# Kernel optimization log

Measured on AMD Instinct MI355X. Metric: run time of the kernel, lower is better.

Reference implementation:

```python
import jax, jax.numpy as jnp
import numpy as np

B, P, O, C = 32, 65536, 32, 2
THRESH = 0.35
VAR = (0.1, 0.2)
LOC_W, LANDM_W = 2.0, 1.0
ALPHA, GAMMA = 0.25, 1.5
EPS = 1e-7


def setup_inputs():
    key = jax.random.key(0)
    k = jax.random.split(key, 8)
    loc_data = jax.random.normal(k[0], (B, P, 4), jnp.float32) * 0.1
    conf_data = jax.random.normal(k[1], (B, P, C), jnp.float32)
    landm_data = jax.random.normal(k[2], (B, P, 10), jnp.float32) * 0.1
    # priors in center form (cx, cy, w, h)
    cxcy = jax.random.uniform(k[3], (P, 2), minval=0.05, maxval=0.95)
    wh = jax.random.uniform(k[4], (P, 2), minval=0.02, maxval=0.3)
    priors = jnp.concatenate([cxcy, wh], axis=-1).astype(jnp.float32)
    # targets [B, O, 15]: corner box (4) + 5 landmarks (10) + label (1, in {-1, +1})
    xy1 = jax.random.uniform(k[5], (B, O, 2), minval=0.0, maxval=0.7)
    bwh = jax.random.uniform(k[6], (B, O, 2), minval=0.05, maxval=0.25)
    boxes = jnp.concatenate([xy1, xy1 + bwh], axis=-1)
    landms = jnp.tile(xy1 + bwh * 0.5, (1, 1, 5))
    labels = (jax.random.randint(k[7], (B, O, 1), 0, 2) * 2 - 1).astype(jnp.float32)
    targets = jnp.concatenate([boxes, landms, labels], axis=-1)
    return {"loc_data": loc_data, "conf_data": conf_data, "landm_data": landm_data,
            "priors": priors, "targets": targets}


def point_form(pr):  # (cx,cy,w,h) -> (x1,y1,x2,y2)
    return jnp.concatenate([pr[:, :2] - pr[:, 2:] / 2, pr[:, :2] + pr[:, 2:] / 2], -1)


def pairwise_iou(a, b):  # a [O,4], b [P,4] corner form -> [O,P]
    lt = jnp.maximum(a[:, None, :2], b[None, :, :2])
    rb = jnp.minimum(a[:, None, 2:], b[None, :, 2:])
    whd = jnp.clip(rb - lt, 0.0)
    inter = whd[..., 0] * whd[..., 1]
    area_a = ((a[:, 2] - a[:, 0]) * (a[:, 3] - a[:, 1]))[:, None]
    area_b = ((b[:, 2] - b[:, 0]) * (b[:, 3] - b[:, 1]))[None, :]
    return inter / (area_a + area_b - inter)


def encode_landm(matched, priors):  # matched [P,10], priors [P,4] center form
    m = matched.reshape(P, 5, 2)
    g = (m - priors[:, None, :2]) / (VAR[0] * priors[:, None, 2:])
    return g.reshape(P, 10)


def match_one(truths, landms, labels, priors_pf, priors):
    ov = pairwise_iou(truths, priors_pf)                       # [O,P]
    best_prior_idx = jnp.argmax(ov, axis=1)                    # [O] best prior per gt
    best_truth_overlap = ov.max(axis=0)                        # [P]
    best_truth_idx = jnp.argmax(ov, axis=0)                    # [P]
    # ensure every gt keeps its best prior
    best_truth_overlap = best_truth_overlap.at[best_prior_idx].set(2.0)
    best_truth_idx = best_truth_idx.at[best_prior_idx].set(jnp.arange(truths.shape[0]))
    loc_t = truths[best_truth_idx]                             # [P,4] matched gt boxes (corner)
    conf = jnp.where(best_truth_overlap < THRESH, 0.0, labels[best_truth_idx])
    landm_t = encode_landm(landms[best_truth_idx], priors)     # [P,10]
    return loc_t, conf, landm_t


def decode(loc, priors):  # SSD center-form decode -> corner boxes
    xy = priors[..., :2] + loc[..., :2] * VAR[0] * priors[..., 2:]
    wh = priors[..., 2:] * jnp.exp(loc[..., 2:] * VAR[1])
    return jnp.concatenate([xy - wh / 2, xy + wh / 2], -1)


def giou(b1, b2):  # elementwise GIoU, corner form
    area1 = (b1[..., 2] - b1[..., 0]) * (b1[..., 3] - b1[..., 1])
    area2 = (b2[..., 2] - b2[..., 0]) * (b2[..., 3] - b2[..., 1])
    iw = jnp.clip(jnp.minimum(b1[..., 2], b2[..., 2]) - jnp.maximum(b1[..., 0], b2[..., 0]), 0.0)
    ih = jnp.clip(jnp.minimum(b1[..., 3], b2[..., 3]) - jnp.maximum(b1[..., 1], b2[..., 1]), 0.0)
    inter = iw * ih
    union = area1 + area2 - inter
    iou = inter / (union + EPS)
    ew = jnp.maximum(b1[..., 2], b2[..., 2]) - jnp.minimum(b1[..., 0], b2[..., 0])
    eh = jnp.maximum(b1[..., 3], b2[..., 3]) - jnp.minimum(b1[..., 1], b2[..., 1])
    enc = ew * eh
    return iou - (enc - union) / (enc + EPS)


def smooth_l1(x):
    ax = jnp.abs(x)
    return jnp.where(ax < 1.0, 0.5 * x * x, ax - 0.5)


def reference(loc_data, conf_data, landm_data, priors, targets):
    # matching uses detached (.data) priors/targets in the original
    priors_c = jax.lax.stop_gradient(priors)
    targets_c = jax.lax.stop_gradient(targets)
    truths, landms, labels = targets_c[..., :4], targets_c[..., 4:14], targets_c[..., 14]
    priors_pf = point_form(priors_c)
    loc_t, conf_raw, landm_t = jax.vmap(match_one, in_axes=(0, 0, 0, None, None))(
        truths, landms, labels, priors_pf, priors_c)  # [B,P,4],[B,P],[B,P,10]

    # landmark loss on pos1 = conf > 0 (label +1: face with landmarks)
    pos1 = conf_raw > 0
    N1 = jnp.maximum(pos1.sum().astype(jnp.float32), 1.0)
    loss_landm = (smooth_l1(landm_data - landm_t).sum(-1) * pos1).sum() * LANDM_W

    # loc GIoU loss on pos = conf != 0
    pos = conf_raw != 0
    conf_t = pos.astype(jnp.int32)  # conf_t[pos] = 1, background 0
    dec = decode(loc_data, priors_c[None])  # [B,P,4]
    loss_l = jnp.where(pos, 1.0 - giou(dec, loc_t), 0.0).sum() * LOC_W

    # focal loss over all B*P anchors (size_average=False -> sum)
    logp = jax.nn.log_softmax(conf_data, axis=-1)
    logp_t = jnp.take_along_axis(logp, conf_t[..., None], axis=-1)[..., 0]
    p_t = jnp.exp(logp_t)
    loss_c = (-ALPHA * (1.0 - p_t) ** GAMMA * logp_t).sum()

    # original normalizes loss_l and loss_c by num_pos_landm sum (N), landm by N1 (==N)
    N = N1
    return (loss_l / N, loss_c / N, loss_landm / N1)
```

## Files before the change

### kernel.cpp

```cpp
#include <hip/hip_runtime.h>
#include <cstdint>

#define B_ 32
#define P_ 65536
#define O_ 32
#define GX_ 64
#define KC_ 4
#define THRESH_ 0.35f
#define VAR0 0.1f
#define VAR1 0.2f
#define EPS_ 1e-7f
#define ALPHA_ 0.25f

struct WSHdr {
  unsigned long long gkey[B_ * O_];
  float4 part[GX_ * B_];
};

__device__ __forceinline__ float frcp(float x) { return __builtin_amdgcn_rcpf(x); }

template <int CTRL>
__device__ __forceinline__ float dpp_fmax(float v) {
  int s = __builtin_amdgcn_update_dpp(0, __float_as_int(v), CTRL, 0xF, 0xF, true);
  return fmaxf(v, __int_as_float(s));
}
template <int CTRL>
__device__ __forceinline__ unsigned dpp_umax(unsigned v) {
  unsigned u = (unsigned)__builtin_amdgcn_update_dpp(0, (int)v, CTRL, 0xF, 0xF, true);
  return u > v ? u : v;
}

__global__ void init_ws(WSHdr* ws) {
  int t = blockIdx.x * blockDim.x + threadIdx.x;
  if (t < B_ * O_) ws->gkey[t] = 0ull;
}

template <bool BIG>
__global__ __launch_bounds__(256) void k_match(const float* __restrict__ priors,
                                               const float* __restrict__ targets,
                                               WSHdr* __restrict__ ws,
                                               uint2* __restrict__ pb) {
  __shared__ float tsh[O_][5];
  __shared__ unsigned long long kq[O_][17];
  const int b = blockIdx.y;
  const int tid = threadIdx.x;
  const int lane = tid & 63, wid = tid >> 6;
  if (tid < O_) {
    const float* trow = targets + ((size_t)b * O_ + tid) * 15;
    float x1 = trow[0], y1 = trow[1], x2 = trow[2], y2 = trow[3];
    tsh[tid][0] = x1; tsh[tid][1] = y1; tsh[tid][2] = x2; tsh[tid][3] = y2;
    tsh[tid][4] = (x2 - x1) * (y2 - y1);
  }
  __syncthreads();

  float px1[KC_], py1[KC_], px2[KC_], py2[KC_], pa[KC_], bov[KC_];
  int bidx[KC_];
  unsigned pinv[KC_];
  #pragma unroll
  for (int k = 0; k < KC_; ++k) {
    unsigned p = (unsigned)((blockIdx.x + k * GX_) * 256 + tid);
    pinv[k] = 0xFFFFFFFFu - p;
    float4 pr = reinterpret_cast<const float4*>(priors)[p];
    px1[k] = pr.x - pr.z * 0.5f; py1[k] = pr.y - pr.w * 0.5f;
    px2[k] = pr.x + pr.z * 0.5f; py2[k] = pr.y + pr.w * 0.5f;
    pa[k] = (px2[k] - px1[k]) * (py2[k] - py1[k]);
    bov[k] = -1.f; bidx[k] = 0;
  }

  #pragma unroll 4
  for (int o = 0; o < O_; ++o) {
    const float x1 = tsh[o][0], y1 = tsh[o][1], x2 = tsh[o][2], y2 = tsh[o][3];
    const float ta = tsh[o][4];
    float tiou = 0.f;
    unsigned tinv = pinv[0];
    #pragma unroll
    for (int k = 0; k < KC_; ++k) {
      float iw = fmaxf(fminf(x2, px2[k]) - fmaxf(x1, px1[k]), 0.f);
      float ih = fmaxf(fminf(y2, py2[k]) - fmaxf(y1, py1[k]), 0.f);
      float inter = iw * ih;
      float iou = inter * frcp(ta + pa[k] - inter);
      if (iou > bov[k]) { bov[k] = iou; bidx[k] = o; }
      if (iou > tiou)   { tiou = iou; tinv = pinv[k]; }
    }
    float m = tiou;
    m = dpp_fmax<0x128>(m);
    m = dpp_fmax<0x124>(m);
    m = dpp_fmax<0x122>(m);
    m = dpp_fmax<0x121>(m);
    unsigned cand = (tiou == m) ? tinv : 0u;
    cand = dpp_umax<0x128>(cand);
    cand = dpp_umax<0x124>(cand);
    cand = dpp_umax<0x122>(cand);
    cand = dpp_umax<0x121>(cand);
    if ((lane & 15) == 0)
      kq[o][wid * 4 + (lane >> 4)] =
          ((unsigned long long)__float_as_uint(m) << 32) | (unsigned long long)cand;
  }

  if (BIG) {
    #pragma unroll
    for (int k = 0; k < KC_; ++k)
      pb[(size_t)b * P_ + (0xFFFFFFFFu - pinv[k])] =
          make_uint2(__float_as_uint(bov[k]), (unsigned)bidx[k]);
  }
  __syncthreads();
  if (tid < O_) {
    unsigned long long best = kq[tid][0];
    #pragma unroll
    for (int s = 1; s < 16; ++s) {
      unsigned long long v = kq[tid][s];
      if (v > best) best = v;
    }
    atomicMax(&ws->gkey[(size_t)b * O_ + tid], best);
  }
}

template <bool BIG>
__global__ __launch_bounds__(256) void k_loss(const float* __restrict__ loc_data,
                                              const float* __restrict__ conf_data,
                                              const float* __restrict__ landm_data,
                                              const float* __restrict__ priors,
                                              const float* __restrict__ targets,
                                              WSHdr* __restrict__ ws,
                                              const uint2* __restrict__ pb) {
  __shared__ float tx1[O_], ty1[O_], tx2[O_], ty2[O_], tarea[O_], tlbl[O_];
  __shared__ float tlm[O_][10];
  __shared__ unsigned fp_s[O_];
  __shared__ unsigned char fmap[KC_ * 256];
  __shared__ float4 wsum[4];
  const int b = blockIdx.y;
  const int tid = threadIdx.x;
  #pragma unroll
  for (int k = 0; k < KC_; ++k) fmap[k * 256 + tid] = 0xFF;
  if (tid < O_) {
    const float* trow = targets + ((size_t)b * O_ + tid) * 15;
    float x1 = trow[0], y1 = trow[1], x2 = trow[2], y2 = trow[3];
    tx1[tid] = x1; ty1[tid] = y1; tx2[tid] = x2; ty2[tid] = y2;
    tarea[tid] = (x2 - x1) * (y2 - y1);
    #pragma unroll
    for (int k = 0; k < 10; ++k) tlm[tid][k] = trow[4 + k];
    tlbl[tid] = trow[14];
    fp_s[tid] = 0xFFFFFFFFu - (unsigned)(ws->gkey[(size_t)b * O_ + tid] & 0xFFFFFFFFull);
  }
  __syncthreads();
  if (tid == 0) {
    for (int j = 0; j < O_; ++j) {
      unsigned fp = fp_s[j];
      unsigned c = fp >> 8;
      if ((c & (GX_ - 1)) == (unsigned)blockIdx.x)
        fmap[(c >> 6) * 256 + (fp & 255)] = (unsigned char)j;
    }
  }
  __syncthreads();

  float vx = 0.f, vy = 0.f, vz = 0.f, vw = 0.f;

  #pragma unroll
  for (int k = 0; k < KC_; ++k) {
    const int p = (blockIdx.x + k * GX_) * 256 + tid;
    const size_t bp = (size_t)b * P_ + p;
    float4 pr = reinterpret_cast<const float4*>(priors)[p];

    float ov;
    int idx;
    if (BIG) {
      uint2 v = pb[bp];
      ov = __uint_as_float(v.x);
      idx = (int)v.y;
    } else {
      float px1 = pr.x - pr.z * 0.5f, py1 = pr.y - pr.w * 0.5f;
      float px2 = pr.x + pr.z * 0.5f, py2 = pr.y + pr.w * 0.5f;
      float parea = (px2 - px1) * (py2 - py1);
      float bov = -1.f;
      int bidx = 0;
      #pragma unroll 8
      for (int o = 0; o < O_; ++o) {
        float iw = fmaxf(fminf(tx2[o], px2) - fmaxf(tx1[o], px1), 0.f);
        float ih = fmaxf(fminf(ty2[o], py2) - fmaxf(ty1[o], py1), 0.f);
        float inter = iw * ih;
        float iou = inter * frcp(tarea[o] + parea - inter);
        if (iou > bov) { bov = iou; bidx = o; }
      }
      ov = bov; idx = bidx;
    }
    unsigned char fj = fmap[k * 256 + tid];
    if (fj != 0xFF) { idx = (int)fj; ov = 2.0f; }

    const bool pos = !(ov < THRESH_);
    const bool pos1 = pos && (tlbl[idx] > 0.f);

    float2 cf = reinterpret_cast<const float2*>(conf_data)[bp];
    float mx = fmaxf(cf.x, cf.y);
    float lse = mx + __logf(1.f + __expf(-fabsf(cf.x - cf.y)));
    float logpt = (pos ? cf.y : cf.x) - lse;
    float pt = __expf(logpt);
    float om = 1.f - pt;
    vy += -ALPHA_ * om * sqrtf(om) * logpt;

    if (pos) {
      float4 loc = reinterpret_cast<const float4*>(loc_data)[bp];
      float dx = pr.x + loc.x * VAR0 * pr.z;
      float dy = pr.y + loc.y * VAR0 * pr.w;
      float dw = pr.z * __expf(loc.z * VAR1);
      float dh = pr.w * __expf(loc.w * VAR1);
      float b1x1 = dx - dw * 0.5f, b1y1 = dy - dh * 0.5f;
      float b1x2 = dx + dw * 0.5f, b1y2 = dy + dh * 0.5f;
      float b2x1 = tx1[idx], b2y1 = ty1[idx], b2x2 = tx2[idx], b2y2 = ty2[idx];
      float a1 = (b1x2 - b1x1) * (b1y2 - b1y1);
      float a2 = (b2x2 - b2x1) * (b2y2 - b2y1);
      float iw = fmaxf(fminf(b1x2, b2x2) - fmaxf(b1x1, b2x1), 0.f);
      float ih = fmaxf(fminf(b1y2, b2y2) - fmaxf(b1y1, b2y1), 0.f);
      float inter = iw * ih;
      float uni = a1 + a2 - inter;
      float iou = inter * frcp(uni + EPS_);
      float ew = fmaxf(b1x2, b2x2) - fminf(b1x1, b2x1);
      float eh = fmaxf(b1y2, b2y2) - fminf(b1y1, b2y1);
      float enc = ew * eh;
      float g = iou - (enc - uni) * frcp(enc + EPS_);
      vx += 1.f - g;
    }
    if (pos1) {
      vw += 1.f;
      const float* lmrow = landm_data + bp * 10;
      float rw = frcp(VAR0 * pr.z);
      float rh = frcp(VAR0 * pr.w);
      float llm = 0.f;
      #pragma unroll
      for (int q = 0; q < 5; ++q) {
        float2 d = *reinterpret_cast<const float2*>(lmrow + q * 2);
        float ex = d.x - (tlm[idx][2 * q] - pr.x) * rw;
        float ey = d.y - (tlm[idx][2 * q + 1] - pr.y) * rh;
        float ax = fabsf(ex), ay = fabsf(ey);
        llm += (ax < 1.f) ? 0.5f * ex * ex : ax - 0.5f;
        llm += (ay < 1.f) ? 0.5f * ey * ey : ay - 0.5f;
      }
      vz += llm;
    }
  }

  #pragma unroll
  for (int i = 32; i > 0; i >>= 1) {
    vx += __shfl_xor(vx, i);
    vy += __shfl_xor(vy, i);
    vz += __shfl_xor(vz, i);
    vw += __shfl_xor(vw, i);
  }
  const int wave = tid >> 6, lane = tid & 63;
  if (lane == 0) wsum[wave] = make_float4(vx, vy, vz, vw);
  __syncthreads();
  if (tid == 0) {
    float sx = 0.f, sy = 0.f, sz = 0.f, sw = 0.f;
    #pragma unroll
    for (int w = 0; w < 4; ++w) {
      sx += wsum[w].x; sy += wsum[w].y; sz += wsum[w].z; sw += wsum[w].w;
    }
    ws->part[(size_t)blockIdx.y * GX_ + blockIdx.x] = make_float4(sx, sy, sz, sw);
  }
}

__global__ __launch_bounds__(256) void k_final(const WSHdr* __restrict__ ws,
                                               float* __restrict__ out) {
  __shared__ double sh[4][4];
  const int tid = threadIdx.x;
  double sx = 0.0, sy = 0.0, sz = 0.0, sw = 0.0;
  for (int i = tid; i < GX_ * B_; i += 256) {
    float4 v = ws->part[i];
    sx += v.x; sy += v.y; sz += v.z; sw += v.w;
  }
  #pragma unroll
  for (int i = 32; i > 0; i >>= 1) {
    sx += __shfl_xor(sx, i);
    sy += __shfl_xor(sy, i);
    sz += __shfl_xor(sz, i);
    sw += __shfl_xor(sw, i);
  }
  const int wave = tid >> 6, lane = tid & 63;
  if (lane == 0) { sh[wave][0] = sx; sh[wave][1] = sy; sh[wave][2] = sz; sh[wave][3] = sw; }
  __syncthreads();
  if (tid == 0) {
    double ax = 0, ay = 0, az = 0, aw = 0;
    #pragma unroll
    for (int w = 0; w < 4; ++w) { ax += sh[w][0]; ay += sh[w][1]; az += sh[w][2]; aw += sh[w][3]; }
    double n1 = aw < 1.0 ? 1.0 : aw;
    out[0] = (float)(2.0 * ax / n1);
    out[1] = (float)(ay / n1);
    out[2] = (float)(az / n1);
  }
}

extern "C" void kernel_launch(void* const* d_in, const int* in_sizes, int n_in,
                              void* d_out, int out_size, void* d_ws, size_t ws_size,
                              hipStream_t stream) {
  (void)in_sizes; (void)n_in; (void)out_size;
  const float* loc     = (const float*)d_in[0];
  const float* conf    = (const float*)d_in[1];
  const float* landm   = (const float*)d_in[2];
  const float* priors  = (const float*)d_in[3];
  const float* targets = (const float*)d_in[4];
  WSHdr* ws = (WSHdr*)d_ws;
  uint2* pb = (uint2*)((char*)d_ws + sizeof(WSHdr));
  float* out = (float*)d_out;
  const bool big = ws_size >= sizeof(WSHdr) + (size_t)B_ * P_ * sizeof(uint2);

  hipLaunchKernelGGL(init_ws, dim3(4), dim3(256), 0, stream, ws);
  dim3 grid(GX_, B_);
  if (big) {
    hipLaunchKernelGGL(k_match<true>, grid, dim3(256), 0, stream, priors, targets, ws, pb);
    hipLaunchKernelGGL(k_loss<true>, grid, dim3(256), 0, stream,
                       loc, conf, landm, priors, targets, ws, pb);
  } else {
    hipLaunchKernelGGL(k_match<false>, grid, dim3(256), 0, stream, priors, targets, ws, pb);
    hipLaunchKernelGGL(k_loss<false>, grid, dim3(256), 0, stream,
                       loc, conf, landm, priors, targets, ws, pb);
  }
  hipLaunchKernelGGL(k_final, dim3(1), dim3(256), 0, stream, ws, out);
}
```

Baseline: 77.00 us.

## Fuse matching and loss kernels, apply forced-match corrections in a small fix-up kernel

Merges the prior-matching and loss computation into one kernel that computes losses using the per-prior best-truth match directly. It no longer writes and re-reads a per-prior match buffer through global memory. A new per-batch kernel then recomputes the up to 32 forced best-prior matches, subtracting their original contribution and adding the forced-positive one as delta corrections. This removes a full pass over intermediate data and one large kernel launch. In exchange it adds a small serial correction kernel and depends on the duplicate-handling logic being right.

After: 73.17 us. 1.05x faster.

```diff
diff --git a/kernel.cpp b/kernel.cpp
--- a/kernel.cpp
+++ b/kernel.cpp
@@ -15,6 +15,7 @@
 struct WSHdr {
   unsigned long long gkey[B_ * O_];
   float4 part[GX_ * B_];
+  double corr[B_][4];
 };
 
 __device__ __forceinline__ float frcp(float x) { return __builtin_amdgcn_rcpf(x); }
@@ -30,18 +31,72 @@
   return u > v ? u : v;
 }
 
+__device__ __forceinline__ float focal_term(float2 cf, bool pos) {
+  float mx = fmaxf(cf.x, cf.y);
+  float lse = mx + __logf(1.f + __expf(-fabsf(cf.x - cf.y)));
+  float logpt = (pos ? cf.y : cf.x) - lse;
+  float pt = __expf(logpt);
+  float om = 1.f - pt;
+  return -ALPHA_ * om * sqrtf(om) * logpt;
+}
+
+__device__ __forceinline__ float giou_term(float4 pr, float4 loc,
+                                           float b2x1, float b2y1,
+                                           float b2x2, float b2y2) {
+  float dx = pr.x + loc.x * VAR0 * pr.z;
+  float dy = pr.y + loc.y * VAR0 * pr.w;
+  float dw = pr.z * __expf(loc.z * VAR1);
+  float dh = pr.w * __expf(loc.w * VAR1);
+  float b1x1 = dx - dw * 0.5f, b1y1 = dy - dh * 0.5f;
+  float b1x2 = dx + dw * 0.5f, b1y2 = dy + dh * 0.5f;
+  float a1 = (b1x2 - b1x1) * (b1y2 - b1y1);
+  float a2 = (b2x2 - b2x1) * (b2y2 - b2y1);
+  float iw = fmaxf(fminf(b1x2, b2x2) - fmaxf(b1x1, b2x1), 0.f);
+  float ih = fmaxf(fminf(b1y2, b2y2) - fmaxf(b1y1, b2y1), 0.f);
+  float inter = iw * ih;
+  float uni = a1 + a2 - inter;
+  float iou = inter * frcp(uni + EPS_);
+  float ew = fmaxf(b1x2, b2x2) - fminf(b1x1, b2x1);
+  float eh = fmaxf(b1y2, b2y2) - fminf(b1y1, b2y1);
+  float enc = ew * eh;
+  float g = iou - (enc - uni) * frcp(enc + EPS_);
+  return 1.f - g;
+}
+
+__device__ __forceinline__ float landm_term(float4 pr,
+                                            const float* __restrict__ lmrow,
+                                            const float* __restrict__ tlm_row) {
+  float rw = frcp(VAR0 * pr.z);
+  float rh = frcp(VAR0 * pr.w);
+  float llm = 0.f;
+  #pragma unroll
+  for (int q = 0; q < 5; ++q) {
+    float2 d = *reinterpret_cast<const float2*>(lmrow + q * 2);
+    float ex = d.x - (tlm_row[2 * q] - pr.x) * rw;
+    float ey = d.y - (tlm_row[2 * q + 1] - pr.y) * rh;
+    float ax = fabsf(ex), ay = fabsf(ey);
+    llm += (ax < 1.f) ? 0.5f * ex * ex : ax - 0.5f;
+    llm += (ay < 1.f) ? 0.5f * ey * ey : ay - 0.5f;
+  }
+  return llm;
+}
+
 __global__ void init_ws(WSHdr* ws) {
   int t = blockIdx.x * blockDim.x + threadIdx.x;
   if (t < B_ * O_) ws->gkey[t] = 0ull;
 }
 
-template <bool BIG>
-__global__ __launch_bounds__(256) void k_match(const float* __restrict__ priors,
+__global__ __launch_bounds__(256) void k_fused(const float* __restrict__ loc_data,
+                                               const float* __restrict__ conf_data,
+                                               const float* __restrict__ landm_data,
+                                               const float* __restrict__ priors,
                                                const float* __restrict__ targets,
-                                               WSHdr* __restrict__ ws,
-                                               uint2* __restrict__ pb) {
+                                               WSHdr* __restrict__ ws) {
   __shared__ float tsh[O_][5];
+  __shared__ float tlbl[O_];
+  __shared__ float tlm[O_][10];
   __shared__ unsigned long long kq[O_][17];
+  __shared__ float4 wsum[4];
   const int b = blockIdx.y;
   const int tid = threadIdx.x;
   const int lane = tid & 63, wid = tid >> 6;
@@ -50,6 +105,9 @@
     float x1 = trow[0], y1 = trow[1], x2 = trow[2], y2 = trow[3];
     tsh[tid][0] = x1; tsh[tid][1] = y1; tsh[tid][2] = x2; tsh[tid][3] = y2;
     tsh[tid][4] = (x2 - x1) * (y2 - y1);
+    #pragma unroll
+    for (int k = 0; k < 10; ++k) tlm[tid][k] = trow[4 + k];
+    tlbl[tid] = trow[14];
   }
   __syncthreads();
 
@@ -97,12 +155,28 @@
           ((unsigned long long)__float_as_uint(m) << 32) | (unsigned long long)cand;
   }
 
-  if (BIG) {
-    #pragma unroll
-    for (int k = 0; k < KC_; ++k)
-      pb[(size_t)b * P_ + (0xFFFFFFFFu - pinv[k])] =
-          make_uint2(__float_as_uint(bov[k]), (unsigned)bidx[k]);
-  }
+  float vx = 0.f, vy = 0.f, vz = 0.f, vw = 0.f;
+  #pragma unroll
+  for (int k = 0; k < KC_; ++k) {
+    const unsigned p = 0xFFFFFFFFu - pinv[k];
+    const size_t bp = (size_t)b * P_ + p;
+    const float ov = bov[k];
+    const int idx = bidx[k];
+    const bool pos = !(ov < THRESH_);
+    const bool pos1 = pos && (tlbl[idx] > 0.f);
+    float2 cf = reinterpret_cast<const float2*>(conf_data)[bp];
+    vy += focal_term(cf, pos);
+    if (pos) {
+      float4 pr = reinterpret_cast<const float4*>(priors)[p];
+      float4 loc = reinterpret_cast<const float4*>(loc_data)[bp];
+      vx += giou_term(pr, loc, tsh[idx][0], tsh[idx][1], tsh[idx][2], tsh[idx][3]);
+      if (pos1) {
+        vw += 1.f;
+        vz += landm_term(pr, landm_data + bp * 10, &tlm[idx][0]);
+      }
+    }
+  }
+
   __syncthreads();
   if (tid < O_) {
     unsigned long long best = kq[tid][0];
@@ -112,130 +186,6 @@
       if (v > best) best = v;
     }
     atomicMax(&ws->gkey[(size_t)b * O_ + tid], best);
-  }
-}
-
-template <bool BIG>
-__global__ __launch_bounds__(256) void k_loss(const float* __restrict__ loc_data,
-                                              const float* __restrict__ conf_data,
-                                              const float* __restrict__ landm_data,
-                                              const float* __restrict__ priors,
-                                              const float* __restrict__ targets,
-                                              WSHdr* __restrict__ ws,
-                                              const uint2* __restrict__ pb) {
-  __shared__ float tx1[O_], ty1[O_], tx2[O_], ty2[O_], tarea[O_], tlbl[O_];
-  __shared__ float tlm[O_][10];
-  __shared__ unsigned fp_s[O_];
-  __shared__ unsigned char fmap[KC_ * 256];
-  __shared__ float4 wsum[4];
-  const int b = blockIdx.y;
-  const int tid = threadIdx.x;
-  #pragma unroll
-  for (int k = 0; k < KC_; ++k) fmap[k * 256 + tid] = 0xFF;
-  if (tid < O_) {
-    const float* trow = targets + ((size_t)b * O_ + tid) * 15;
-    float x1 = trow[0], y1 = trow[1], x2 = trow[2], y2 = trow[3];
-    tx1[tid] = x1; ty1[tid] = y1; tx2[tid] = x2; ty2[tid] = y2;
-    tarea[tid] = (x2 - x1) * (y2 - y1);
-    #pragma unroll
-    for (int k = 0; k < 10; ++k) tlm[tid][k] = trow[4 + k];
-    tlbl[tid] = trow[14];
-    fp_s[tid] = 0xFFFFFFFFu - (unsigned)(ws->gkey[(size_t)b * O_ + tid] & 0xFFFFFFFFull);
-  }
-  __syncthreads();
-  if (tid == 0) {
-    for (int j = 0; j < O_; ++j) {
-      unsigned fp = fp_s[j];
-      unsigned c = fp >> 8;
-      if ((c & (GX_ - 1)) == (unsigned)blockIdx.x)
-        fmap[(c >> 6) * 256 + (fp & 255)] = (unsigned char)j;
-    }
-  }
-  __syncthreads();
-
-  float vx = 0.f, vy = 0.f, vz = 0.f, vw = 0.f;
-
-  #pragma unroll
-  for (int k = 0; k < KC_; ++k) {
-    const int p = (blockIdx.x + k * GX_) * 256 + tid;
-    const size_t bp = (size_t)b * P_ + p;
-    float4 pr = reinterpret_cast<const float4*>(priors)[p];
-
-    float ov;
-    int idx;
-    if (BIG) {
-      uint2 v = pb[bp];
-      ov = __uint_as_float(v.x);
-      idx = (int)v.y;
-    } else {
-      float px1 = pr.x - pr.z * 0.5f, py1 = pr.y - pr.w * 0.5f;
-      float px2 = pr.x + pr.z * 0.5f, py2 = pr.y + pr.w * 0.5f;
-      float parea = (px2 - px1) * (py2 - py1);
-      float bov = -1.f;
-      int bidx = 0;
-      #pragma unroll 8
-      for (int o = 0; o < O_; ++o) {
-        float iw = fmaxf(fminf(tx2[o], px2) - fmaxf(tx1[o], px1), 0.f);
-        float ih = fmaxf(fminf(ty2[o], py2) - fmaxf(ty1[o], py1), 0.f);
-        float inter = iw * ih;
-        float iou = inter * frcp(tarea[o] + parea - inter);
-        if (iou > bov) { bov = iou; bidx = o; }
-      }
-      ov = bov; idx = bidx;
-    }
-    unsigned char fj = fmap[k * 256 + tid];
-    if (fj != 0xFF) { idx = (int)fj; ov = 2.0f; }
-
-    const bool pos = !(ov < THRESH_);
-    const bool pos1 = pos && (tlbl[idx] > 0.f);
-
-    float2 cf = reinterpret_cast<const float2*>(conf_data)[bp];
-    float mx = fmaxf(cf.x, cf.y);
-    float lse = mx + __logf(1.f + __expf(-fabsf(cf.x - cf.y)));
-    float logpt = (pos ? cf.y : cf.x) - lse;
-    float pt = __expf(logpt);
-    float om = 1.f - pt;
-    vy += -ALPHA_ * om * sqrtf(om) * logpt;
-
-    if (pos) {
-      float4 loc = reinterpret_cast<const float4*>(loc_data)[bp];
-      float dx = pr.x + loc.x * VAR0 * pr.z;
-      float dy = pr.y + loc.y * VAR0 * pr.w;
-      float dw = pr.z * __expf(loc.z * VAR1);
-      float dh = pr.w * __expf(loc.w * VAR1);
-      float b1x1 = dx - dw * 0.5f, b1y1 = dy - dh * 0.5f;
-      float b1x2 = dx + dw * 0.5f, b1y2 = dy + dh * 0.5f;
-      float b2x1 = tx1[idx], b2y1 = ty1[idx], b2x2 = tx2[idx], b2y2 = ty2[idx];
-      float a1 = (b1x2 - b1x1) * (b1y2 - b1y1);
-      float a2 = (b2x2 - b2x1) * (b2y2 - b2y1);
-      float iw = fmaxf(fminf(b1x2, b2x2) - fmaxf(b1x1, b2x1), 0.f);
-      float ih = fmaxf(fminf(b1y2, b2y2) - fmaxf(b1y1, b2y1), 0.f);
-      float inter = iw * ih;
-      float uni = a1 + a2 - inter;
-      float iou = inter * frcp(uni + EPS_);
-      float ew = fmaxf(b1x2, b2x2) - fminf(b1x1, b2x1);
-      float eh = fmaxf(b1y2, b2y2) - fminf(b1y1, b2y1);
-      float enc = ew * eh;
-      float g = iou - (enc - uni) * frcp(enc + EPS_);
-      vx += 1.f - g;
-    }
-    if (pos1) {
-      vw += 1.f;
-      const float* lmrow = landm_data + bp * 10;
-      float rw = frcp(VAR0 * pr.z);
-      float rh = frcp(VAR0 * pr.w);
-      float llm = 0.f;
-      #pragma unroll
-      for (int q = 0; q < 5; ++q) {
-        float2 d = *reinterpret_cast<const float2*>(lmrow + q * 2);
-        float ex = d.x - (tlm[idx][2 * q] - pr.x) * rw;
-        float ey = d.y - (tlm[idx][2 * q + 1] - pr.y) * rh;
-        float ax = fabsf(ex), ay = fabsf(ey);
-        llm += (ax < 1.f) ? 0.5f * ex * ex : ax - 0.5f;
-        llm += (ay < 1.f) ? 0.5f * ey * ey : ay - 0.5f;
-      }
-      vz += llm;
-    }
   }
 
   #pragma unroll
@@ -245,8 +195,7 @@
     vz += __shfl_xor(vz, i);
     vw += __shfl_xor(vw, i);
   }
-  const int wave = tid >> 6, lane = tid & 63;
-  if (lane == 0) wsum[wave] = make_float4(vx, vy, vz, vw);
+  if (lane == 0) wsum[wid] = make_float4(vx, vy, vz, vw);
   __syncthreads();
   if (tid == 0) {
     float sx = 0.f, sy = 0.f, sz = 0.f, sw = 0.f;
@@ -255,6 +204,97 @@
       sx += wsum[w].x; sy += wsum[w].y; sz += wsum[w].z; sw += wsum[w].w;
     }
     ws->part[(size_t)blockIdx.y * GX_ + blockIdx.x] = make_float4(sx, sy, sz, sw);
+  }
+}
+
+__global__ __launch_bounds__(64) void k_fix(const float* __restrict__ loc_data,
+                                            const float* __restrict__ conf_data,
+                                            const float* __restrict__ landm_data,
+                                            const float* __restrict__ priors,
+                                            const float* __restrict__ targets,
+                                            WSHdr* __restrict__ ws) {
+  __shared__ float tsh[O_][5];
+  __shared__ float tlbl[O_];
+  __shared__ float tlm[O_][10];
+  const int b = blockIdx.x;
+  const int tid = threadIdx.x;
+  if (tid < O_) {
+    const float* trow = targets + ((size_t)b * O_ + tid) * 15;
+    float x1 = trow[0], y1 = trow[1], x2 = trow[2], y2 = trow[3];
+    tsh[tid][0] = x1; tsh[tid][1] = y1; tsh[tid][2] = x2; tsh[tid][3] = y2;
+    tsh[tid][4] = (x2 - x1) * (y2 - y1);
+    #pragma unroll
+    for (int k = 0; k < 10; ++k) tlm[tid][k] = trow[4 + k];
+    tlbl[tid] = trow[14];
+  }
+  __syncthreads();
+
+  unsigned fp = 0xFFFFFFFFu;
+  if (tid < O_)
+    fp = 0xFFFFFFFFu - (unsigned)(ws->gkey[(size_t)b * O_ + tid] & 0xFFFFFFFFull);
+  bool alive = tid < O_;
+  for (int j2 = 0; j2 < O_; ++j2) {
+    unsigned f2 = __shfl(fp, j2, 64);
+    if (j2 > tid && f2 == fp) alive = false;
+  }
+
+  float dll = 0.f, dlc = 0.f, dllm = 0.f, dn1 = 0.f;
+  if (alive) {
+    const int p = (int)fp;
+    const size_t bp = (size_t)b * P_ + p;
+    float4 pr = reinterpret_cast<const float4*>(priors)[p];
+    float px1 = pr.x - pr.z * 0.5f, py1 = pr.y - pr.w * 0.5f;
+    float px2 = pr.x + pr.z * 0.5f, py2 = pr.y + pr.w * 0.5f;
+    float pa = (px2 - px1) * (py2 - py1);
+    float bov = -1.f;
+    int bidx = 0;
+    for (int o = 0; o < O_; ++o) {
+      const float x1 = tsh[o][0], y1 = tsh[o][1], x2 = tsh[o][2], y2 = tsh[o][3];
+      const float ta = tsh[o][4];
+      float iw = fmaxf(fminf(x2, px2) - fmaxf(x1, px1), 0.f);
+      float ih = fmaxf(fminf(y2, py2) - fmaxf(y1, py1), 0.f);
+      float inter = iw * ih;
+      float iou = inter * frcp(ta + pa - inter);
+      if (iou > bov) { bov = iou; bidx = o; }
+    }
+    float2 cf = reinterpret_cast<const float2*>(conf_data)[bp];
+    float4 loc = reinterpret_cast<const float4*>(loc_data)[bp];
+    const float* lmrow = landm_data + bp * 10;
+    {
+      const bool pos = !(bov < THRESH_);
+      const bool pos1 = pos && (tlbl[bidx] > 0.f);
+      dlc -= focal_term(cf, pos);
+      if (pos) {
+        dll -= giou_term(pr, loc, tsh[bidx][0], tsh[bidx][1], tsh[bidx][2], tsh[bidx][3]);
+        if (pos1) {
+          dn1 -= 1.f;
+          dllm -= landm_term(pr, lmrow, &tlm[bidx][0]);
+        }
+      }
+    }
+    {
+      const int idx = tid;
+      const bool pos1 = tlbl[idx] > 0.f;
+      dlc += focal_term(cf, true);
+      dll += giou_term(pr, loc, tsh[idx][0], tsh[idx][1], tsh[idx][2], tsh[idx][3]);
+      if (pos1) {
+        dn1 += 1.f;
+        dllm += landm_term(pr, lmrow, &tlm[idx][0]);
+      }
+    }
+  }
+  #pragma unroll
+  for (int i = 32; i > 0; i >>= 1) {
+    dll += __shfl_xor(dll, i);
+    dlc += __shfl_xor(dlc, i);
+    dllm += __shfl_xor(dllm, i);
+    dn1 += __shfl_xor(dn1, i);
+  }
+  if (tid == 0) {
+    ws->corr[b][0] = (double)dll;
+    ws->corr[b][1] = (double)dlc;
+    ws->corr[b][2] = (double)dllm;
+    ws->corr[b][3] = (double)dn1;
   }
 }
 
@@ -267,6 +307,12 @@
     float4 v = ws->part[i];
     sx += v.x; sy += v.y; sz += v.z; sw += v.w;
   }
+  if (tid < B_) {
+    sx += ws->corr[tid][0];
+    sy += ws->corr[tid][1];
+    sz += ws->corr[tid][2];
+    sw += ws->corr[tid][3];
+  }
   #pragma unroll
   for (int i = 32; i > 0; i >>= 1) {
     sx += __shfl_xor(sx, i);
@@ -291,27 +337,19 @@
 extern "C" void kernel_launch(void* const* d_in, const int* in_sizes, int n_in,
                               void* d_out, int out_size, void* d_ws, size_t ws_size,
                               hipStream_t stream) {
-  (void)in_sizes; (void)n_in; (void)out_size;
+  (void)in_sizes; (void)n_in; (void)out_size; (void)ws_size;
   const float* loc     = (const float*)d_in[0];
   const float* conf    = (const float*)d_in[1];
   const float* landm   = (const float*)d_in[2];
   const float* priors  = (const float*)d_in[3];
   const float* targets = (const float*)d_in[4];
   WSHdr* ws = (WSHdr*)d_ws;
-  uint2* pb = (uint2*)((char*)d_ws + sizeof(WSHdr));
   float* out = (float*)d_out;
-  const bool big = ws_size >= sizeof(WSHdr) + (size_t)B_ * P_ * sizeof(uint2);
 
   hipLaunchKernelGGL(init_ws, dim3(4), dim3(256), 0, stream, ws);
-  dim3 grid(GX_, B_);
-  if (big) {
-    hipLaunchKernelGGL(k_match<true>, grid, dim3(256), 0, stream, priors, targets, ws, pb);
-    hipLaunchKernelGGL(k_loss<true>, grid, dim3(256), 0, stream,
-                       loc, conf, landm, priors, targets, ws, pb);
-  } else {
-    hipLaunchKernelGGL(k_match<false>, grid, dim3(256), 0, stream, priors, targets, ws, pb);
-    hipLaunchKernelGGL(k_loss<false>, grid, dim3(256), 0, stream,
-                       loc, conf, landm, priors, targets, ws, pb);
-  }
+  hipLaunchKernelGGL(k_fused, dim3(GX_, B_), dim3(256), 0, stream,
+                     loc, conf, landm, priors, targets, ws);
+  hipLaunchKernelGGL(k_fix, dim3(B_), dim3(64), 0, stream,
+                     loc, conf, landm, priors, targets, ws);
   hipLaunchKernelGGL(k_final, dim3(1), dim3(256), 0, stream, ws, out);
 }
```
